# Performance work log

Measured on AMD Instinct MI355X. Metric: run time of the kernel, lower is better.

The kernel has to match this reference:

```python
import jax, jax.numpy as jnp
import numpy as np

D, H, K = 384, 6, 8
B, NQ, NK = 4, 2048, 2048
EPS = 1e-5


def _ln(x, s, b):
    m = jnp.mean(x, axis=-1, keepdims=True)
    v = jnp.mean((x - m) ** 2, axis=-1, keepdims=True)
    return (x - m) * jax.lax.rsqrt(v + EPS) * s + b


def _mha(q, k, v, Wo, bo):
    # q,k,v: [B, N, D]
    dh = D // H
    qh = q.reshape(q.shape[0], q.shape[1], H, dh).transpose(0, 2, 1, 3)
    kh = k.reshape(k.shape[0], k.shape[1], H, dh).transpose(0, 2, 1, 3)
    vh = v.reshape(v.shape[0], v.shape[1], H, dh).transpose(0, 2, 1, 3)
    scores = jnp.einsum('bhqd,bhkd->bhqk', qh, kh) / jnp.sqrt(jnp.asarray(dh, q.dtype))
    attn = jax.nn.softmax(scores, axis=-1)
    out = jnp.einsum('bhqk,bhkd->bhqd', attn, vh)
    out = out.transpose(0, 2, 1, 3).reshape(q.shape[0], q.shape[1], D)
    return out @ Wo + bo


def _knn_edge(q_coords, k_coords, q_feats, k_feats):
    # coords: [B, N, 3]; feats: [B, N, D]. EdgeConv-style feature:
    # concat(neighbor_feat - center_feat, center_feat) -> [B, Nq, K, 2D]
    d2 = (jnp.sum(q_coords ** 2, -1)[:, :, None]
          + jnp.sum(k_coords ** 2, -1)[:, None, :]
          - 2.0 * jnp.einsum('bqc,bkc->bqk', q_coords, k_coords))
    _, idx = jax.lax.top_k(-d2, K)  # [B, Nq, K] nearest neighbors in key set
    neigh = jax.vmap(lambda f, i: f[i])(k_feats, idx)  # [B, Nq, K, D]
    center = jnp.broadcast_to(q_feats[:, :, None, :], neigh.shape)
    return jnp.concatenate([neigh - center, center], axis=-1)


def setup_inputs() -> dict:
    key = jax.random.key(0)
    ks = jax.random.split(key, 24)
    s = 0.02
    return {
        'query_points': jax.random.normal(ks[0], (B, 3 + D, NQ), jnp.float32),
        'key_points': jax.random.normal(ks[1], (B, 3 + D, NK), jnp.float32),
        'ln_in_s': jnp.ones((D,), jnp.float32), 'ln_in_b': jnp.zeros((D,), jnp.float32),
        'qkv_W': jax.random.normal(ks[2], (D, 3 * D), jnp.float32) * s,
        'attn_out_W': jax.random.normal(ks[3], (D, D), jnp.float32) * s,
        'attn_out_b': jnp.zeros((D,), jnp.float32),
        'ff_W1': jax.random.normal(ks[4], (D, 2 * D), jnp.float32) * s,
        'ff_b1': jnp.zeros((2 * D,), jnp.float32),
        'ff_W2': jax.random.normal(ks[5], (2 * D, D), jnp.float32) * s,
        'ff_b2': jnp.zeros((D,), jnp.float32),
        'ffn_s': jnp.ones((D,), jnp.float32), 'ffn_b': jnp.zeros((D,), jnp.float32),
        'knn1_W': jax.random.normal(ks[6], (2 * D, D), jnp.float32) * s,
        'knn1_b': jnp.zeros((D,), jnp.float32),
        'knn2_W': jax.random.normal(ks[7], (2 * D, D), jnp.float32) * s,
        'knn2_b': jnp.zeros((D,), jnp.float32),
        'self_merge_W': jax.random.normal(ks[8], (2 * D, D), jnp.float32) * s,
        'self_merge_b': jnp.zeros((D,), jnp.float32),
        'cross_merge_W': jax.random.normal(ks[9], (2 * D, D), jnp.float32) * s,
        'cross_merge_b': jnp.zeros((D,), jnp.float32),
        'cnq_s': jnp.ones((D,), jnp.float32), 'cnq_b': jnp.zeros((D,), jnp.float32),
        'cnk_s': jnp.ones((D,), jnp.float32), 'cnk_b': jnp.zeros((D,), jnp.float32),
        'cq_W': jax.random.normal(ks[10], (D, D), jnp.float32) * s,
        'ck_W': jax.random.normal(ks[11], (D, D), jnp.float32) * s,
        'cv_W': jax.random.normal(ks[12], (D, D), jnp.float32) * s,
    }


def reference(query_points, key_points, ln_in_s, ln_in_b, qkv_W, attn_out_W,
              attn_out_b, ff_W1, ff_b1, ff_W2, ff_b2, ffn_s, ffn_b,
              knn1_W, knn1_b, knn2_W, knn2_b, self_merge_W, self_merge_b,
              cross_merge_W, cross_merge_b, cnq_s, cnq_b, cnk_s, cnk_b,
              cq_W, ck_W, cv_W):
    qp = jnp.transpose(query_points, (0, 2, 1))  # [B, Nq, 3+D]
    kp = jnp.transpose(key_points, (0, 2, 1))    # [B, Nk, 3+D]
    q_coords, q_feats = qp[..., :3], qp[..., 3:]
    k_coords, k_feats = kp[..., :3], kp[..., 3:]

    # --- self attention + self kNN geometry ---
    norm_f = _ln(q_feats, ln_in_s, ln_in_b)
    qkv = norm_f @ qkv_W
    q, k, v = jnp.split(qkv, 3, axis=-1)
    attn_f = _mha(q, k, v, attn_out_W, attn_out_b)

    edge = _knn_edge(q_coords, q_coords, norm_f, norm_f)          # [B,Nq,K,2D]
    geom = jax.nn.leaky_relu(edge @ knn1_W + knn1_b, 0.2)
    geom = jnp.max(geom, axis=2)                                   # [B,Nq,D]

    attn_f = jnp.concatenate([attn_f, geom], axis=-1) @ self_merge_W + self_merge_b
    q_feats = attn_f + q_feats

    # --- cross attention + cross kNN geometry ---
    nq = _ln(q_feats, cnq_s, cnq_b)
    nk = _ln(k_feats, cnk_s, cnk_b)
    cross_f = _mha(nq @ cq_W, nk @ ck_W, nk @ cv_W, attn_out_W, attn_out_b)

    cedge = _knn_edge(q_coords, k_coords, nq, nk)                  # [B,Nq,K,2D]
    cgeom = jax.nn.leaky_relu(cedge @ knn2_W + knn2_b, 0.2)
    cgeom = jnp.max(cgeom, axis=2)

    cross_f = jnp.concatenate([cross_f, cgeom], axis=-1) @ cross_merge_W + cross_merge_b
    q_feats = q_feats + cross_f

    # --- feed forward ---
    h = _ln(q_feats, ffn_s, ffn_b)
    q_feats = q_feats + (jax.nn.gelu(h @ ff_W1 + ff_b1) @ ff_W2 + ff_b2)

    out = jnp.concatenate([q_coords, q_feats], axis=-1)
    return jnp.transpose(out, (0, 2, 1))  # [B, 3+D, Nq]
```

## Files before the change

kernel.cpp:

```cpp
#include <hip/hip_runtime.h>
#include <cstdint>
#include <cstddef>

#define NB 4
#define NN 2048
#define DD 384
#define NH 6

typedef float f4 __attribute__((ext_vector_type(4)));
typedef float f32x4 __attribute__((ext_vector_type(4)));
typedef short bf16x8 __attribute__((ext_vector_type(8)));
typedef unsigned u32x2 __attribute__((ext_vector_type(2)));

__device__ __forceinline__ float gelu_t(float x) {
  float x3 = x*x*x;
  return 0.5f*x*(1.0f + tanhf(0.7978845608028654f*(x + 0.044715f*x3)));
}

__device__ __forceinline__ unsigned short f2b(float f) {
  unsigned u = __builtin_bit_cast(unsigned, f);
  u += 0x7fffu + ((u >> 16) & 1u);
  return (unsigned short)(u >> 16);
}

__device__ __forceinline__ float b2f(unsigned short u) {
  return __builtin_bit_cast(float, ((unsigned)u) << 16);
}

__device__ __forceinline__ unsigned cvtpk(float a, float b) {
  unsigned r;
  asm("v_cvt_pk_bf16_f32 %0, %1, %2" : "=v"(r) : "v"(a), "v"(b));
  return r;
}

typedef __attribute__((address_space(1))) const void gvoid_t;
typedef __attribute__((address_space(3))) void lvoid_t;
__device__ __forceinline__ void gl16(const void* g, void* l) {
  __builtin_amdgcn_global_load_lds((gvoid_t*)g, (lvoid_t*)l, 16, 0, 0);
}

__device__ __forceinline__ unsigned long long shfl_xor_u64(unsigned long long v, int m) {
  unsigned lo = (unsigned)v, hi = (unsigned)(v >> 32);
  lo = (unsigned)__shfl_xor((int)lo, m);
  hi = (unsigned)__shfl_xor((int)hi, m);
  return ((unsigned long long)hi << 32) | lo;
}

__global__ __launch_bounds__(256) void split_k(const float* __restrict__ pts,
                                               float* __restrict__ coords,
                                               float* __restrict__ feats) {
  __shared__ float t[32][33];
  int b = blockIdx.z;
  int c0 = blockIdx.x*32, n0 = blockIdx.y*32;
  int tx = threadIdx.x, ty = threadIdx.y;
#pragma unroll
  for (int i = 0; i < 4; ++i) {
    int c = c0 + ty + i*8;
    if (c < 387) t[ty+i*8][tx] = pts[((size_t)b*387 + c)*NN + n0 + tx];
  }
  __syncthreads();
#pragma unroll
  for (int i = 0; i < 4; ++i) {
    int n = n0 + ty + i*8;
    int c = c0 + tx;
    if (c < 387) {
      float v = t[tx][ty+i*8];
      if (c < 3) coords[((size_t)b*NN + n)*4 + c] = v;
      else       feats[((size_t)b*NN + n)*DD + (c-3)] = v;
    }
  }
}

__global__ __launch_bounds__(256) void kprep_k(float* __restrict__ c4) {
  int i = blockIdx.x*256 + threadIdx.x;
  f4 v = *(f4*)(c4 + (size_t)i*4);
  v[3] = v[0]*v[0] + v[1]*v[1] + v[2]*v[2];
  *(f4*)(c4 + (size_t)i*4) = v;
}

__global__ __launch_bounds__(256) void pack_k(const float* __restrict__ coords,
                                              const float* __restrict__ feats,
                                              float* __restrict__ out) {
  __shared__ float t[32][33];
  int b = blockIdx.z;
  int c0 = blockIdx.x*32, n0 = blockIdx.y*32;
  int tx = threadIdx.x, ty = threadIdx.y;
#pragma unroll
  for (int i = 0; i < 4; ++i) {
    int n = n0 + ty + i*8;
    int c = c0 + tx;
    if (c < 387) {
      float v = (c < 3) ? coords[((size_t)b*NN + n)*4 + c]
                        : feats[((size_t)b*NN + n)*DD + (c-3)];
      t[tx][ty+i*8] = v;
    }
  }
  __syncthreads();
#pragma unroll
  for (int i = 0; i < 4; ++i) {
    int c = c0 + ty + i*8;
    if (c < 387) out[((size_t)b*387 + c)*NN + n0 + tx] = t[ty+i*8][tx];
  }
}

__device__ __forceinline__ void ln_body(const float* __restrict__ x,
                                        const float* __restrict__ g,
                                        const float* __restrict__ bb,
                                        unsigned short* __restrict__ o,
                                        int row) {
  int lane = threadIdx.x & 63;
  const float* xr = x + (size_t)row*DD;
  float v[6]; float s = 0.f;
#pragma unroll
  for (int i = 0; i < 6; ++i) { v[i] = xr[lane + i*64]; s += v[i]; }
#pragma unroll
  for (int off = 1; off < 64; off <<= 1) s += __shfl_xor(s, off);
  float mean = s * (1.f/384.f);
  float s2 = 0.f;
#pragma unroll
  for (int i = 0; i < 6; ++i) { float d = v[i] - mean; s2 += d*d; }
#pragma unroll
  for (int off = 1; off < 64; off <<= 1) s2 += __shfl_xor(s2, off);
  float rs = rsqrtf(s2*(1.f/384.f) + 1e-5f);
  unsigned short* orow = o + (size_t)row*DD;
#pragma unroll
  for (int i = 0; i < 6; ++i) {
    int c = lane + i*64;
    orow[c] = f2b((v[i]-mean)*rs*g[c] + bb[c]);
  }
}

__global__ __launch_bounds__(256) void ln_k(const float* __restrict__ x,
                                            const float* __restrict__ g,
                                            const float* __restrict__ bb,
                                            unsigned short* __restrict__ o) {
  ln_body(x, g, bb, o, blockIdx.x*4 + (threadIdx.x >> 6));
}

__global__ __launch_bounds__(256) void ln2_k(const float* __restrict__ x1,
                                             const float* __restrict__ g1,
                                             const float* __restrict__ b1,
                                             unsigned short* __restrict__ o1,
                                             const float* __restrict__ x2,
                                             const float* __restrict__ g2,
                                             const float* __restrict__ b2,
                                             unsigned short* __restrict__ o2) {
  int row = blockIdx.x*4 + (threadIdx.x >> 6);
  if (blockIdx.y == 0) ln_body(x1, g1, b1, o1, row);
  else                 ln_body(x2, g2, b2, o2, row);
}

struct WSrcs { const float* p[13]; };

__global__ __launch_bounds__(256) void wtrans_k(WSrcs srcs, unsigned short* __restrict__ dst) {
  constexpr int KK[13]  = {384,384,384,384,768,384,384,384,384,384,768,384,768};
  constexpr int NW[13]  = {1152,384,384,384,384,384,384,384,384,384,384,768,384};
  constexpr int MD[13]  = {0,0,2,0,0,0,0,0,0,2,0,0,0};
  constexpr int OFF[13] = {0,442368,589824,737280,884736,1179648,1327104,1474560,
                           1622016,1769472,1916928,2211840,2506752};
  constexpr int PFX[14] = {0,432,576,720,864,1152,1296,1440,1584,1728,1872,2160,2448,2736};
  int bid = blockIdx.x;
  int e = 0;
  while (bid >= PFX[e+1]) ++e;
  int t = bid - PFX[e];
  int K = KK[e], N = NW[e];
  int ntiles = N >> 5;
  int kt = t / ntiles, nt = t - kt*ntiles;
  const float* src = srcs.p[e];
  __shared__ float T[32][33];
  int tx = threadIdx.x & 31, ty = threadIdx.x >> 5;
  int n = nt*32 + tx;
#pragma unroll
  for (int i = 0; i < 4; ++i) {
    int k = kt*32 + ty + i*8;
    float v = src[(size_t)k*N + n];
    if (MD[e] == 2) v = src[(size_t)(k+384)*N + n] - v;
    T[ty+i*8][tx] = v;
  }
  __syncthreads();
#pragma unroll
  for (int i = 0; i < 4; ++i) {
    int nn = nt*32 + ty + i*8;
    int kk = kt*32 + tx;
    dst[(size_t)OFF[e] + (size_t)nn*K + kk] = f2b(T[tx][ty+i*8]);
  }
}

template<int ACT, int ACC, int OB, int HALFM>
__global__ __launch_bounds__(256) void mgemm_k(const unsigned short* __restrict__ A, int lda,
                                               const unsigned short* __restrict__ Wt,
                                               const float* __restrict__ bias,
                                               void* __restrict__ Cv, int ldc, int cofs,
                                               int Kd) {
  constexpr int BM   = HALFM ? 64 : 128;
  constexpr int MT   = HALFM ? 2 : 4;
  constexpr int AG   = HALFM ? 2 : 4;
  constexpr int ABUF = BM*128;
  constexpr int BUFSZ = ABUF + 8192;
  __shared__ char lds[2*BUFSZ];
  int tid = threadIdx.x;
  int lane = tid & 63, w = tid >> 6, g = lane >> 4, c = lane & 15;
  int wr = w >> 1, wc = w & 1;
  int m0 = blockIdx.y*BM, n0 = blockIdx.x*64;
  int lrow = lane >> 3;
  int cswz = ((lane & 7) ^ lrow)*8;

  f32x4 acc[MT][2];
#pragma unroll
  for (int mt = 0; mt < MT; ++mt)
#pragma unroll
    for (int nt = 0; nt < 2; ++nt) acc[mt][nt] = 0.f;

  int KT = Kd >> 6;
  {
    char* As = lds; char* Bs = lds + ABUF;
#pragma unroll
    for (int i = 0; i < AG; ++i) {
      int rb = i*32 + w*8;
      gl16(A + (size_t)(m0 + rb + lrow)*lda + cswz, As + rb*128);
    }
#pragma unroll
    for (int i = 0; i < 2; ++i) {
      int rb = i*32 + w*8;
      gl16(Wt + (size_t)(n0 + rb + lrow)*Kd + cswz, Bs + rb*128);
    }
  }
  __syncthreads();

  for (int kt = 0; kt < KT; ++kt) {
    char* Asc = lds + (kt & 1)*BUFSZ;
    char* Bsc = Asc + ABUF;
    if (kt + 1 < KT) {
      char* Asn = lds + ((kt + 1) & 1)*BUFSZ;
      char* Bsn = Asn + ABUF;
      int k0 = (kt + 1)*64;
#pragma unroll
      for (int i = 0; i < AG; ++i) {
        int rb = i*32 + w*8;
        gl16(A + (size_t)(m0 + rb + lrow)*lda + k0 + cswz, Asn + rb*128);
      }
#pragma unroll
      for (int i = 0; i < 2; ++i) {
        int rb = i*32 + w*8;
        gl16(Wt + (size_t)(n0 + rb + lrow)*Kd + k0 + cswz, Bsn + rb*128);
      }
    }
#pragma unroll
    for (int kb = 0; kb < 2; ++kb) {
      bf16x8 af[MT], bfr[2];
#pragma unroll
      for (int mt = 0; mt < MT; ++mt) {
        int row = wr*(BM/2) + mt*16 + c;
        int ch = (kb*4 + g) ^ (row & 7);
        af[mt] = *(const bf16x8*)(Asc + row*128 + ch*16);
      }
#pragma unroll
      for (int nt = 0; nt < 2; ++nt) {
        int row = wc*32 + nt*16 + c;
        int ch = (kb*4 + g) ^ (row & 7);
        bfr[nt] = *(const bf16x8*)(Bsc + row*128 + ch*16);
      }
#pragma unroll
      for (int mt = 0; mt < MT; ++mt)
#pragma unroll
        for (int nt = 0; nt < 2; ++nt)
          acc[mt][nt] = __builtin_amdgcn_mfma_f32_16x16x32_bf16(af[mt], bfr[nt], acc[mt][nt], 0, 0, 0);
    }
    __syncthreads();
  }

#pragma unroll
  for (int mt = 0; mt < MT; ++mt) {
#pragma unroll
    for (int nt = 0; nt < 2; ++nt) {
      int coln = n0 + wc*32 + nt*16 + c;
      float bval = bias ? bias[coln] : 0.f;
#pragma unroll
      for (int r = 0; r < 4; ++r) {
        int m = m0 + wr*(BM/2) + mt*16 + 4*g + r;
        float t = acc[mt][nt][r] + bval;
        if (ACT == 1) t = gelu_t(t);
        if (OB) {
          ((unsigned short*)Cv)[(size_t)m*ldc + cofs + coln] = f2b(t);
        } else {
          float* cp = (float*)Cv + (size_t)m*ldc + cofs + coln;
          if (ACC) t += *cp;
          *cp = t;
        }
      }
    }
  }
}

struct FSegs {
  const unsigned short* A[5];
  unsigned short* out[5];
  int ldc[5];
  int cofs[5];
};

__global__ __launch_bounds__(256) void fgemm_k(FSegs fs, const unsigned short* __restrict__ Wt) {
  __shared__ char lds[49152];
  int tid = threadIdx.x;
  int lane = tid & 63, w = tid >> 6, g = lane >> 4, c = lane & 15;
  int wr = w >> 1, wc = w & 1;
  int m0 = blockIdx.y*128, n0 = blockIdx.x*64;
  int seg = n0 / 384;
  const unsigned short* A = fs.A[seg];
  int lrow = lane >> 3;
  int cswz = ((lane & 7) ^ lrow)*8;

  f32x4 acc[4][2];
#pragma unroll
  for (int mt = 0; mt < 4; ++mt)
#pragma unroll
    for (int nt = 0; nt < 2; ++nt) acc[mt][nt] = 0.f;

  {
    char* As = lds; char* Bs = lds + 16384;
#pragma unroll
    for (int i = 0; i < 4; ++i) {
      int rb = i*32 + w*8;
      gl16(A + (size_t)(m0 + rb + lrow)*384 + cswz, As + rb*128);
    }
#pragma unroll
    for (int i = 0; i < 2; ++i) {
      int rb = i*32 + w*8;
      gl16(Wt + (size_t)(n0 + rb + lrow)*384 + cswz, Bs + rb*128);
    }
  }
  __syncthreads();

  for (int kt = 0; kt < 6; ++kt) {
    char* Asc = lds + (kt & 1)*24576;
    char* Bsc = Asc + 16384;
    if (kt + 1 < 6) {
      char* Asn = lds + ((kt + 1) & 1)*24576;
      char* Bsn = Asn + 16384;
      int k0 = (kt + 1)*64;
#pragma unroll
      for (int i = 0; i < 4; ++i) {
        int rb = i*32 + w*8;
        gl16(A + (size_t)(m0 + rb + lrow)*384 + k0 + cswz, Asn + rb*128);
      }
#pragma unroll
      for (int i = 0; i < 2; ++i) {
        int rb = i*32 + w*8;
        gl16(Wt + (size_t)(n0 + rb + lrow)*384 + k0 + cswz, Bsn + rb*128);
      }
    }
#pragma unroll
    for (int kb = 0; kb < 2; ++kb) {
      bf16x8 af[4], bfr[2];
#pragma unroll
      for (int mt = 0; mt < 4; ++mt) {
        int row = wr*64 + mt*16 + c;
        int ch = (kb*4 + g) ^ (row & 7);
        af[mt] = *(const bf16x8*)(Asc + row*128 + ch*16);
      }
#pragma unroll
      for (int nt = 0; nt < 2; ++nt) {
        int row = wc*32 + nt*16 + c;
        int ch = (kb*4 + g) ^ (row & 7);
        bfr[nt] = *(const bf16x8*)(Bsc + row*128 + ch*16);
      }
#pragma unroll
      for (int mt = 0; mt < 4; ++mt)
#pragma unroll
        for (int nt = 0; nt < 2; ++nt)
          acc[mt][nt] = __builtin_amdgcn_mfma_f32_16x16x32_bf16(af[mt], bfr[nt], acc[mt][nt], 0, 0, 0);
    }
    __syncthreads();
  }

  if (seg == 2) {
    unsigned short* vtp = fs.out[2];
    int bb = m0 >> 11;
    int tokb = (m0 & 2047) + wr*64 + 4*g;
#pragma unroll
    for (int mt = 0; mt < 4; ++mt) {
#pragma unroll
      for (int nt = 0; nt < 2; ++nt) {
        int cseg = (n0 - 768) + wc*32 + nt*16 + c;
        int h = cseg >> 6, d = cseg & 63;
        u32x2 pv;
        pv[0] = cvtpk(acc[mt][nt][0], acc[mt][nt][1]);
        pv[1] = cvtpk(acc[mt][nt][2], acc[mt][nt][3]);
        *(u32x2*)(vtp + ((size_t)((bb*NH + h)*64 + d))*NN + tokb + mt*16) = pv;
      }
    }
    return;
  }

  unsigned short* outp = fs.out[seg];
  int ldcs = fs.ldc[seg];
  int cbase = fs.cofs[seg] + (n0 - seg*384);
#pragma unroll
  for (int mt = 0; mt < 4; ++mt) {
#pragma unroll
    for (int nt = 0; nt < 2; ++nt) {
      int coln = cbase + wc*32 + nt*16 + c;
#pragma unroll
      for (int r = 0; r < 4; ++r) {
        int m = m0 + wr*64 + mt*16 + 4*g + r;
        outp[(size_t)m*ldcs + coln] = f2b(acc[mt][nt][r]);
      }
    }
  }
}

__global__ __launch_bounds__(256) void flashm_k(const unsigned short* __restrict__ qkvb,
                                                const unsigned short* __restrict__ vt,
                                                unsigned short* __restrict__ o) {
  __shared__ char smem[40960];
  char* PT = smem + 32768;
  int bid = blockIdx.x;
  int s = (bid & 7)*96 + (bid >> 3);
  int qt = s & 31; int hb = s >> 5;
  int h = hb % NH, b = hb / NH;
  int q0 = qt*64;
  int tid = threadIdx.x;
  int w = tid >> 6, lane = tid & 63, g = lane >> 4, c = lane & 15;
  int lrow = lane >> 3;
  int gsw = ((lane & 7) ^ lrow)*8;

  const unsigned short* kbase = qkvb + (size_t)b*NN*1152 + 384 + h*64;
  const unsigned short* vbase = vt + ((size_t)(b*NH + h))*64*NN;

  bf16x8 qf[2];
  {
    const unsigned short* qrow = qkvb + ((size_t)(b*NN + q0 + w*16 + c))*1152 + h*64;
    qf[0] = *(const bf16x8*)(qrow + 8*g);
    qf[1] = *(const bf16x8*)(qrow + 32 + 8*g);
  }
  f32x4 oacc[4];
#pragma unroll
  for (int i = 0; i < 4; ++i) oacc[i] = 0.f;
  float lsum = 0.f;

#define FSTAGE(bf, ktb) { \
    char* KB = smem + (bf)*16384; char* VB = KB + 8192; \
    gl16(kbase + (size_t)((ktb) + w*16 + lrow)*1152 + gsw,     KB + (w*16)*128); \
    gl16(kbase + (size_t)((ktb) + w*16 + 8 + lrow)*1152 + gsw, KB + (w*16+8)*128); \
    gl16(vbase + (size_t)(w*16 + lrow)*NN + (ktb) + gsw,       VB + (w*16)*128); \
    gl16(vbase + (size_t)(w*16 + 8 + lrow)*NN + (ktb) + gsw,   VB + (w*16+8)*128); }

  FSTAGE(0, 0);
  __syncthreads();

  for (int kt = 0; kt < 32; ++kt) {
    if (kt + 1 < 32) FSTAGE((kt + 1) & 1, (kt + 1)*64);
    char* KTc = smem + (kt & 1)*16384;
    char* VTc = KTc + 8192;

    f32x4 sT[4];
#pragma unroll
    for (int nt = 0; nt < 4; ++nt) sT[nt] = 0.f;
#pragma unroll
    for (int nt = 0; nt < 4; ++nt) {
      int krow = nt*16 + c;
#pragma unroll
      for (int kb = 0; kb < 2; ++kb) {
        int ch = ((kb*4 + g) ^ (krow & 7))*16;
        bf16x8 kf_ = *(const bf16x8*)(KTc + krow*128 + ch);
        sT[nt] = __builtin_amdgcn_mfma_f32_16x16x32_bf16(kf_, qf[kb], sT[nt], 0, 0, 0);
      }
    }

    int prow = w*16 + c;
    int pswz = (c & 7) << 4;
#pragma unroll
    for (int nt = 0; nt < 4; ++nt) {
      float p0 = __builtin_amdgcn_exp2f(sT[nt][0] * 0.18033688011112042f);
      float p1 = __builtin_amdgcn_exp2f(sT[nt][1] * 0.18033688011112042f);
      float p2 = __builtin_amdgcn_exp2f(sT[nt][2] * 0.18033688011112042f);
      float p3 = __builtin_amdgcn_exp2f(sT[nt][3] * 0.18033688011112042f);
      lsum += (p0 + p1) + (p2 + p3);
      u32x2 pk;
      pk[0] = cvtpk(p0, p1);
      pk[1] = cvtpk(p2, p3);
      *(u32x2*)(PT + prow*128 + ((nt*32 + 8*g) ^ pswz)) = pk;
    }

    bf16x8 pb[2];
#pragma unroll
    for (int kb = 0; kb < 2; ++kb)
      pb[kb] = *(const bf16x8*)(PT + prow*128 + (((kb*4 + g) ^ (c & 7))*16));

#pragma unroll
    for (int dt = 0; dt < 4; ++dt) {
      int vrow = dt*16 + c;
#pragma unroll
      for (int kb = 0; kb < 2; ++kb) {
        int ch = ((kb*4 + g) ^ (vrow & 7))*16;
        bf16x8 vf = *(const bf16x8*)(VTc + vrow*128 + ch);
        oacc[dt] = __builtin_amdgcn_mfma_f32_16x16x32_bf16(vf, pb[kb], oacc[dt], 0, 0, 0);
      }
    }
    __syncthreads();
  }
#undef FSTAGE

  lsum += __shfl_xor(lsum, 16);
  lsum += __shfl_xor(lsum, 32);
  float inv = 1.f / lsum;
  size_t orow = ((size_t)b*NN + q0 + w*16 + c)*DD + h*64;
#pragma unroll
  for (int dt = 0; dt < 4; ++dt) {
    u32x2 ov;
    ov[0] = cvtpk(oacc[dt][0]*inv, oacc[dt][1]*inv);
    ov[1] = cvtpk(oacc[dt][2]*inv, oacc[dt][3]*inv);
    *(u32x2*)(o + orow + dt*16 + 4*g) = ov;
  }
}

#define CEXF(a, b) { \
  float lo_ = fminf(bf[a], bf[b]); \
  float hi_ = fmaxf(bf[a], bf[b]); \
  bf[a] = lo_; bf[b] = hi_; }

#define CEX(a, b) { \
  unsigned long long lo_ = bd[a] < bd[b] ? bd[a] : bd[b]; \
  unsigned long long hi_ = bd[a] < bd[b] ? bd[b] : bd[a]; \
  bd[a] = lo_; bd[b] = hi_; }

__global__ __launch_bounds__(256) void knn2_k(const float* __restrict__ qc4,
                                              const float* __restrict__ kc4,
                                              int* __restrict__ idx1,
                                              int* __restrict__ idx2) {
  const float* kcs = blockIdx.y ? kc4 : qc4;
  int* idxo = blockIdx.y ? idx2 : idx1;
  int lane = threadIdx.x & 63;
  int q = blockIdx.x*4 + (threadIdx.x >> 6);
  int b = q >> 11;
  f4 qv = *(const f4*)(qc4 + (size_t)q*4);
  float mx_ = -2.f*qv[0], my_ = -2.f*qv[1], mz_ = -2.f*qv[2];
  const float* kb = kcs + (size_t)b*NN*4;

  float fv[32];
  float bf[8];
#pragma unroll
  for (int i = 0; i < 8; ++i) bf[i] = INFINITY;
#pragma unroll
  for (int i = 0; i < 32; ++i) {
    f4 kv = *(const f4*)(kb + (size_t)(lane + i*64)*4);
    float f = fmaf(mx_, kv[0], fmaf(my_, kv[1], fmaf(mz_, kv[2], kv[3])));
    fv[i] = f;
#pragma unroll
    for (int k = 0; k < 8; ++k) {
      float lo = fminf(f, bf[k]);
      float hi = fmaxf(f, bf[k]);
      bf[k] = lo; f = hi;
    }
  }
#pragma unroll
  for (int m = 1; m <= 32; m <<= 1) {
    float pr[8];
#pragma unroll
    for (int i = 0; i < 8; ++i) pr[i] = __shfl_xor(bf[7-i], m);
#pragma unroll
    for (int i = 0; i < 8; ++i) bf[i] = fminf(bf[i], pr[i]);
    CEXF(0,4) CEXF(1,5) CEXF(2,6) CEXF(3,7)
    CEXF(0,2) CEXF(1,3) CEXF(4,6) CEXF(5,7)
    CEXF(0,1) CEXF(2,3) CEXF(4,5) CEXF(6,7)
  }
  float T = bf[7];

  unsigned long long bd[8];
#pragma unroll
  for (int i = 0; i < 8; ++i) bd[i] = ~0ull;
#pragma unroll
  for (int i = 0; i < 32; ++i) {
    if (__any(fv[i] <= T)) {
      unsigned u = __builtin_bit_cast(unsigned, fv[i]);
      u ^= 0x80000000u | (unsigned)((int)u >> 31);
      unsigned long long key = ((unsigned long long)u << 32) | (unsigned)(lane + i*64);
#pragma unroll
      for (int k = 0; k < 8; ++k) {
        unsigned long long lo = key < bd[k] ? key : bd[k];
        unsigned long long hi = key < bd[k] ? bd[k] : key;
        bd[k] = lo; key = hi;
      }
    }
  }
#pragma unroll
  for (int m = 1; m <= 32; m <<= 1) {
    unsigned long long pr[8];
#pragma unroll
    for (int i = 0; i < 8; ++i) pr[i] = shfl_xor_u64(bd[7-i], m);
#pragma unroll
    for (int i = 0; i < 8; ++i) bd[i] = bd[i] < pr[i] ? bd[i] : pr[i];
    CEX(0,4) CEX(1,5) CEX(2,6) CEX(3,7)
    CEX(0,2) CEX(1,3) CEX(4,6) CEX(5,7)
    CEX(0,1) CEX(2,3) CEX(4,5) CEX(6,7)
  }
  if (lane == 0) {
#pragma unroll
    for (int r = 0; r < 8; ++r) idxo[(size_t)q*8 + r] = (int)(unsigned)bd[r];
  }
}

__global__ __launch_bounds__(384) void geom_k(const unsigned short* __restrict__ GCb,
                                              const float* __restrict__ bias,
                                              const int* __restrict__ idx,
                                              unsigned short* __restrict__ out) {
  int q = blockIdx.x;
  int b = q >> 11;
  int d = threadIdx.x;
  float c = b2f(GCb[(size_t)q*768 + 384 + d]) + bias[d];
  float mx = -INFINITY;
#pragma unroll
  for (int kn = 0; kn < 8; ++kn) {
    int j = idx[(size_t)q*8 + kn];
    float gg = b2f(GCb[((size_t)(b << 11) + j)*768 + d]);
    float y = gg + c;
    y = (y > 0.f) ? y : 0.2f*y;
    mx = fmaxf(mx, y);
  }
  out[(size_t)q*768 + 384 + d] = f2b(mx);
}

extern "C" void kernel_launch(void* const* d_in, const int* in_sizes, int n_in,
                              void* d_out, int out_size, void* d_ws, size_t ws_size,
                              hipStream_t stream) {
  (void)in_sizes; (void)n_in; (void)out_size; (void)ws_size;
  const float* qpts  = (const float*)d_in[0];
  const float* kpts  = (const float*)d_in[1];
  const float* ln_s  = (const float*)d_in[2];
  const float* ln_b  = (const float*)d_in[3];
  const float* qkvW  = (const float*)d_in[4];
  const float* Wo    = (const float*)d_in[5];
  const float* bo    = (const float*)d_in[6];
  const float* ffW1  = (const float*)d_in[7];
  const float* ffb1  = (const float*)d_in[8];
  const float* ffW2  = (const float*)d_in[9];
  const float* ffb2  = (const float*)d_in[10];
  const float* ffns  = (const float*)d_in[11];
  const float* ffnb  = (const float*)d_in[12];
  const float* knn1W = (const float*)d_in[13];
  const float* knn1b = (const float*)d_in[14];
  const float* knn2W = (const float*)d_in[15];
  const float* knn2b = (const float*)d_in[16];
  const float* smW   = (const float*)d_in[17];
  const float* smb   = (const float*)d_in[18];
  const float* cmW   = (const float*)d_in[19];
  const float* cmb   = (const float*)d_in[20];
  const float* cnqs  = (const float*)d_in[21];
  const float* cnqb  = (const float*)d_in[22];
  const float* cnks  = (const float*)d_in[23];
  const float* cnkb  = (const float*)d_in[24];
  const float* cqW   = (const float*)d_in[25];
  const float* ckW   = (const float*)d_in[26];
  const float* cvW   = (const float*)d_in[27];

  float* ws = (float*)d_ws;
  float* qc4  = ws;
  float* kc4  = qc4 + 32768;
  float* qf   = kc4 + 32768;
  float* kf   = qf + 3145728;
  unsigned short* nrmb = (unsigned short*)(kf + 3145728);
  unsigned short* nkb  = (unsigned short*)(kf + 3145728 + 1572864);
  float* qkv = kf + 3145728 + 1572864 + 1572864;
  unsigned short* qkvb   = (unsigned short*)qkv;
  unsigned short* attnGb = (unsigned short*)qkv;
  unsigned short* vtb    = (unsigned short*)(qkv + 4718592);
  unsigned short* wtb    = (unsigned short*)(qkv + 4718592 + 1572864);
  unsigned short* attnOb = (unsigned short*)(qkv + 4718592 + 1572864 + 1400832);
  unsigned short* GCbb   = (unsigned short*)((float*)attnOb + 1572864);
  int* idx1 = (int*)((float*)GCbb + 3145728);
  int* idx2 = idx1 + 65536;

  const int W_FA=0, W_WO=737280, W_SM=884736, W_FB=1179648,
            W_CM=1916928, W_FF1=2211840, W_FF2=2506752;

  WSrcs srcs;
  srcs.p[0]=qkvW; srcs.p[1]=knn1W; srcs.p[2]=knn1W; srcs.p[3]=Wo; srcs.p[4]=smW;
  srcs.p[5]=cqW; srcs.p[6]=ckW; srcs.p[7]=cvW; srcs.p[8]=knn2W; srcs.p[9]=knn2W;
  srcs.p[10]=cmW; srcs.p[11]=ffW1; srcs.p[12]=ffW2;
  wtrans_k<<<2736, 256, 0, stream>>>(srcs, wtb);

  dim3 tgrid(13, 64, NB), tblk(32, 8);
  split_k<<<tgrid, tblk, 0, stream>>>(qpts, qc4, qf);
  split_k<<<tgrid, tblk, 0, stream>>>(kpts, kc4, kf);
  kprep_k<<<64, 256, 0, stream>>>(qc4);

  knn2_k<<<dim3(2048, 2), 256, 0, stream>>>(qc4, kc4, idx1, idx2);

  dim3 mg384h(6, 128), mg768(12, 64), fg(30, 64);

  ln_k<<<2048, 256, 0, stream>>>(qf, ln_s, ln_b, nrmb);
  {
    FSegs fa;
    for (int s = 0; s < 5; ++s) fa.A[s] = nrmb;
    fa.out[0] = qkvb; fa.ldc[0] = 1152; fa.cofs[0] = 0;
    fa.out[1] = qkvb; fa.ldc[1] = 1152; fa.cofs[1] = 384;
    fa.out[2] = vtb;  fa.ldc[2] = 0;    fa.cofs[2] = 0;
    fa.out[3] = GCbb; fa.ldc[3] = 768;  fa.cofs[3] = 0;
    fa.out[4] = GCbb; fa.ldc[4] = 768;  fa.cofs[4] = 384;
    fgemm_k<<<fg, 256, 0, stream>>>(fa, wtb + W_FA);
  }
  flashm_k<<<768, 256, 0, stream>>>(qkvb, vtb, attnOb);
  mgemm_k<0,0,1,1><<<mg384h, 256, 0, stream>>>(attnOb, DD, wtb+W_WO, bo, attnGb, 768, 0, DD);
  geom_k<<<8192, 384, 0, stream>>>(GCbb, knn1b, idx1, attnGb);
  mgemm_k<0,1,0,1><<<mg384h, 256, 0, stream>>>(attnGb, 768, wtb+W_SM, smb, qf, DD, 0, 768);

  ln2_k<<<dim3(2048, 2), 256, 0, stream>>>(qf, cnqs, cnqb, nrmb, kf, cnks, cnkb, nkb);
  {
    FSegs fb;
    fb.A[0] = nrmb; fb.A[1] = nkb; fb.A[2] = nkb; fb.A[3] = nkb; fb.A[4] = nrmb;
    fb.out[0] = qkvb; fb.ldc[0] = 1152; fb.cofs[0] = 0;
    fb.out[1] = qkvb; fb.ldc[1] = 1152; fb.cofs[1] = 384;
    fb.out[2] = vtb;  fb.ldc[2] = 0;    fb.cofs[2] = 0;
    fb.out[3] = GCbb; fb.ldc[3] = 768;  fb.cofs[3] = 0;
    fb.out[4] = GCbb; fb.ldc[4] = 768;  fb.cofs[4] = 384;
    fgemm_k<<<fg, 256, 0, stream>>>(fb, wtb + W_FB);
  }
  flashm_k<<<768, 256, 0, stream>>>(qkvb, vtb, attnOb);
  mgemm_k<0,0,1,1><<<mg384h, 256, 0, stream>>>(attnOb, DD, wtb+W_WO, bo, attnGb, 768, 0, DD);
  geom_k<<<8192, 384, 0, stream>>>(GCbb, knn2b, idx2, attnGb);
  mgemm_k<0,1,0,1><<<mg384h, 256, 0, stream>>>(attnGb, 768, wtb+W_CM, cmb, qf, DD, 0, 768);

  ln_k<<<2048, 256, 0, stream>>>(qf, ffns, ffnb, nrmb);
  mgemm_k<1,0,1,0><<<mg768, 256, 0, stream>>>(nrmb, DD, wtb+W_FF1, ffb1, attnGb, 768, 0, DD);
  mgemm_k<0,1,0,1><<<mg384h, 256, 0, stream>>>(attnGb, 768, wtb+W_FF2, ffb2, qf, DD, 0, 768);

  pack_k<<<tgrid, tblk, 0, stream>>>(qc4, qf, (float*)d_out);
}
```

Before: 352.1 us.

## Co-schedule kNN with fused GEMM and Wo-GEMM with geometry gather in shared launches

Folds the coordinate squared-norm prep into the split kernel. Merges the kNN search blocks into the first fused projection GEMM launch, and the output-projection GEMM with the edge-geometry max-gather, using interleaved block-index dispatch. The goal is fewer launches and letting independent latency-bound and compute-bound work overlap on the GPU. The cost is larger LDS per block for the kNN and geometry blocks, which may lower their occupancy. The geometry body now runs on 256 threads covering 384 channels, so some threads do a second pass.

```diff
diff --git a/kernel.cpp b/kernel.cpp
--- a/kernel.cpp
+++ b/kernel.cpp
@@ -68,14 +68,11 @@
       if (c < 3) coords[((size_t)b*NN + n)*4 + c] = v;
       else       feats[((size_t)b*NN + n)*DD + (c-3)] = v;
     }
-  }
-}
-
-__global__ __launch_bounds__(256) void kprep_k(float* __restrict__ c4) {
-  int i = blockIdx.x*256 + threadIdx.x;
-  f4 v = *(f4*)(c4 + (size_t)i*4);
-  v[3] = v[0]*v[0] + v[1]*v[1] + v[2]*v[2];
-  *(f4*)(c4 + (size_t)i*4) = v;
+    if (c0 == 0 && tx == 3) {
+      float x = t[0][ty+i*8], y = t[1][ty+i*8], z = t[2][ty+i*8];
+      coords[((size_t)b*NN + n)*4 + 3] = x*x + y*y + z*z;
+    }
+  }
 }
 
 __global__ __launch_bounds__(256) void pack_k(const float* __restrict__ coords,
@@ -187,21 +184,20 @@
 }
 
 template<int ACT, int ACC, int OB, int HALFM>
-__global__ __launch_bounds__(256) void mgemm_k(const unsigned short* __restrict__ A, int lda,
-                                               const unsigned short* __restrict__ Wt,
-                                               const float* __restrict__ bias,
-                                               void* __restrict__ Cv, int ldc, int cofs,
-                                               int Kd) {
+__device__ __forceinline__ void mgemm_body(const unsigned short* __restrict__ A, int lda,
+                                           const unsigned short* __restrict__ Wt,
+                                           const float* __restrict__ bias,
+                                           void* __restrict__ Cv, int ldc, int cofs,
+                                           int Kd, int bx, int by, char* lds) {
   constexpr int BM   = HALFM ? 64 : 128;
   constexpr int MT   = HALFM ? 2 : 4;
   constexpr int AG   = HALFM ? 2 : 4;
   constexpr int ABUF = BM*128;
   constexpr int BUFSZ = ABUF + 8192;
-  __shared__ char lds[2*BUFSZ];
   int tid = threadIdx.x;
   int lane = tid & 63, w = tid >> 6, g = lane >> 4, c = lane & 15;
   int wr = w >> 1, wc = w & 1;
-  int m0 = blockIdx.y*BM, n0 = blockIdx.x*64;
+  int m0 = by*BM, n0 = bx*64;
   int lrow = lane >> 3;
   int cswz = ((lane & 7) ^ lrow)*8;
 
@@ -292,6 +288,18 @@
   }
 }
 
+template<int ACT, int ACC, int OB, int HALFM>
+__global__ __launch_bounds__(256) void mgemm_k(const unsigned short* __restrict__ A, int lda,
+                                               const unsigned short* __restrict__ Wt,
+                                               const float* __restrict__ bias,
+                                               void* __restrict__ Cv, int ldc, int cofs,
+                                               int Kd) {
+  constexpr int BM = HALFM ? 64 : 128;
+  __shared__ char lds[2*(BM*128 + 8192)];
+  mgemm_body<ACT,ACC,OB,HALFM>(A, lda, Wt, bias, Cv, ldc, cofs, Kd,
+                               blockIdx.x, blockIdx.y, lds);
+}
+
 struct FSegs {
   const unsigned short* A[5];
   unsigned short* out[5];
@@ -299,12 +307,12 @@
   int cofs[5];
 };
 
-__global__ __launch_bounds__(256) void fgemm_k(FSegs fs, const unsigned short* __restrict__ Wt) {
-  __shared__ char lds[49152];
+__device__ __forceinline__ void fgemm_body(const FSegs& fs, const unsigned short* __restrict__ Wt,
+                                           int bx, int by, char* lds) {
   int tid = threadIdx.x;
   int lane = tid & 63, w = tid >> 6, g = lane >> 4, c = lane & 15;
   int wr = w >> 1, wc = w & 1;
-  int m0 = blockIdx.y*128, n0 = blockIdx.x*64;
+  int m0 = by*128, n0 = bx*64;
   int seg = n0 / 384;
   const unsigned short* A = fs.A[seg];
   int lrow = lane >> 3;
@@ -407,6 +415,171 @@
       }
     }
   }
+}
+
+__global__ __launch_bounds__(256) void fgemm_k(FSegs fs, const unsigned short* __restrict__ Wt) {
+  __shared__ char lds[49152];
+  fgemm_body(fs, Wt, blockIdx.x, blockIdx.y, lds);
+}
+
+#define CEXF(a, b) { \
+  float lo_ = fminf(bf[a], bf[b]); \
+  float hi_ = fmaxf(bf[a], bf[b]); \
+  bf[a] = lo_; bf[b] = hi_; }
+
+#define CEX(a, b) { \
+  unsigned long long lo_ = bd[a] < bd[b] ? bd[a] : bd[b]; \
+  unsigned long long hi_ = bd[a] < bd[b] ? bd[b] : bd[a]; \
+  bd[a] = lo_; bd[b] = hi_; }
+
+__device__ void knn_body(const float* __restrict__ qc4,
+                         const float* __restrict__ kcs,
+                         int* __restrict__ idxo, int bx) {
+  int lane = threadIdx.x & 63;
+  int q = bx*4 + (threadIdx.x >> 6);
+  int b = q >> 11;
+  f4 qv = *(const f4*)(qc4 + (size_t)q*4);
+  float mx_ = -2.f*qv[0], my_ = -2.f*qv[1], mz_ = -2.f*qv[2];
+  const float* kb = kcs + (size_t)b*NN*4;
+
+  float fv[32];
+  float bf[8];
+#pragma unroll
+  for (int i = 0; i < 8; ++i) bf[i] = INFINITY;
+#pragma unroll
+  for (int i = 0; i < 32; ++i) {
+    f4 kv = *(const f4*)(kb + (size_t)(lane + i*64)*4);
+    float f = fmaf(mx_, kv[0], fmaf(my_, kv[1], fmaf(mz_, kv[2], kv[3])));
+    fv[i] = f;
+#pragma unroll
+    for (int k = 0; k < 8; ++k) {
+      float lo = fminf(f, bf[k]);
+      float hi = fmaxf(f, bf[k]);
+      bf[k] = lo; f = hi;
+    }
+  }
+#pragma unroll
+  for (int m = 1; m <= 32; m <<= 1) {
+    float pr[8];
+#pragma unroll
+    for (int i = 0; i < 8; ++i) pr[i] = __shfl_xor(bf[7-i], m);
+#pragma unroll
+    for (int i = 0; i < 8; ++i) bf[i] = fminf(bf[i], pr[i]);
+    CEXF(0,4) CEXF(1,5) CEXF(2,6) CEXF(3,7)
+    CEXF(0,2) CEXF(1,3) CEXF(4,6) CEXF(5,7)
+    CEXF(0,1) CEXF(2,3) CEXF(4,5) CEXF(6,7)
+  }
+  float T = bf[7];
+
+  unsigned long long bd[8];
+#pragma unroll
+  for (int i = 0; i < 8; ++i) bd[i] = ~0ull;
+#pragma unroll
+  for (int i = 0; i < 32; ++i) {
+    if (__any(fv[i] <= T)) {
+      unsigned u = __builtin_bit_cast(unsigned, fv[i]);
+      u ^= 0x80000000u | (unsigned)((int)u >> 31);
+      unsigned long long key = ((unsigned long long)u << 32) | (unsigned)(lane + i*64);
+#pragma unroll
+      for (int k = 0; k < 8; ++k) {
+        unsigned long long lo = key < bd[k] ? key : bd[k];
+        unsigned long long hi = key < bd[k] ? bd[k] : key;
+        bd[k] = lo; key = hi;
+      }
+    }
+  }
+#pragma unroll
+  for (int m = 1; m <= 32; m <<= 1) {
+    unsigned long long pr[8];
+#pragma unroll
+    for (int i = 0; i < 8; ++i) pr[i] = shfl_xor_u64(bd[7-i], m);
+#pragma unroll
+    for (int i = 0; i < 8; ++i) bd[i] = bd[i] < pr[i] ? bd[i] : pr[i];
+    CEX(0,4) CEX(1,5) CEX(2,6) CEX(3,7)
+    CEX(0,2) CEX(1,3) CEX(4,6) CEX(5,7)
+    CEX(0,1) CEX(2,3) CEX(4,5) CEX(6,7)
+  }
+  if (lane == 0) {
+#pragma unroll
+    for (int r = 0; r < 8; ++r) idxo[(size_t)q*8 + r] = (int)(unsigned)bd[r];
+  }
+}
+
+__global__ __launch_bounds__(256) void fgknn_k(FSegs fs, const unsigned short* __restrict__ Wt,
+                                               const float* __restrict__ qc4,
+                                               const float* __restrict__ kc4,
+                                               int* __restrict__ idx1,
+                                               int* __restrict__ idx2) {
+  __shared__ char lds[49152];
+  int bid = blockIdx.x;
+  int kb;
+  if (bid < 5760) {
+    int t = bid / 3, r = bid - t*3;
+    if (r == 0) { fgemm_body(fs, Wt, t % 30, t / 30, lds); return; }
+    kb = t*2 + (r - 1);
+  } else {
+    kb = 3840 + (bid - 5760);
+  }
+  knn_body(qc4, (kb >= 2048) ? kc4 : qc4, (kb >= 2048) ? idx2 : idx1, kb & 2047);
+}
+
+__device__ __forceinline__ void geom_body(const unsigned short* __restrict__ GCb,
+                                          const float* __restrict__ bias,
+                                          const int* __restrict__ idx,
+                                          unsigned short* __restrict__ out,
+                                          int q) {
+  int b = q >> 11;
+  int t = threadIdx.x;
+  int j[8];
+#pragma unroll
+  for (int k = 0; k < 8; ++k) j[k] = idx[(size_t)q*8 + k];
+  const unsigned short* base = GCb + ((size_t)(b << 11))*768;
+  {
+    float c = b2f(GCb[(size_t)q*768 + 384 + t]) + bias[t];
+    float mx = -INFINITY;
+#pragma unroll
+    for (int k = 0; k < 8; ++k) {
+      float y = b2f(base[(size_t)j[k]*768 + t]) + c;
+      y = (y > 0.f) ? y : 0.2f*y;
+      mx = fmaxf(mx, y);
+    }
+    out[(size_t)q*768 + 384 + t] = f2b(mx);
+  }
+  if (t < 128) {
+    int d = t + 256;
+    float c = b2f(GCb[(size_t)q*768 + 384 + d]) + bias[d];
+    float mx = -INFINITY;
+#pragma unroll
+    for (int k = 0; k < 8; ++k) {
+      float y = b2f(base[(size_t)j[k]*768 + d]) + c;
+      y = (y > 0.f) ? y : 0.2f*y;
+      mx = fmaxf(mx, y);
+    }
+    out[(size_t)q*768 + 384 + d] = f2b(mx);
+  }
+}
+
+__global__ __launch_bounds__(256) void wog_k(const unsigned short* __restrict__ A,
+                                             const unsigned short* __restrict__ Wt,
+                                             const float* __restrict__ wob,
+                                             unsigned short* __restrict__ attnG,
+                                             const unsigned short* __restrict__ GCb,
+                                             const float* __restrict__ gbias,
+                                             const int* __restrict__ idx) {
+  __shared__ char lds[32768];
+  int bid = blockIdx.x;
+  int gq;
+  if (bid < 8448) {
+    int t = bid / 11, r = bid - t*11;
+    if (r == 0) {
+      mgemm_body<0,0,1,1>(A, 384, Wt, wob, attnG, 768, 0, 384, t % 6, t / 6, lds);
+      return;
+    }
+    gq = t*10 + (r - 1);
+  } else {
+    gq = 7680 + (bid - 8448);
+  }
+  geom_body(GCb, gbias, idx, attnG, gq);
 }
 
 __global__ __launch_bounds__(256) void flashm_k(const unsigned short* __restrict__ qkvb,
@@ -512,112 +685,6 @@
     ov[1] = cvtpk(oacc[dt][2]*inv, oacc[dt][3]*inv);
     *(u32x2*)(o + orow + dt*16 + 4*g) = ov;
   }
-}
-
-#define CEXF(a, b) { \
-  float lo_ = fminf(bf[a], bf[b]); \
-  float hi_ = fmaxf(bf[a], bf[b]); \
-  bf[a] = lo_; bf[b] = hi_; }
-
-#define CEX(a, b) { \
-  unsigned long long lo_ = bd[a] < bd[b] ? bd[a] : bd[b]; \
-  unsigned long long hi_ = bd[a] < bd[b] ? bd[b] : bd[a]; \
-  bd[a] = lo_; bd[b] = hi_; }
-
-__global__ __launch_bounds__(256) void knn2_k(const float* __restrict__ qc4,
-                                              const float* __restrict__ kc4,
-                                              int* __restrict__ idx1,
-                                              int* __restrict__ idx2) {
-  const float* kcs = blockIdx.y ? kc4 : qc4;
-  int* idxo = blockIdx.y ? idx2 : idx1;
-  int lane = threadIdx.x & 63;
-  int q = blockIdx.x*4 + (threadIdx.x >> 6);
-  int b = q >> 11;
-  f4 qv = *(const f4*)(qc4 + (size_t)q*4);
-  float mx_ = -2.f*qv[0], my_ = -2.f*qv[1], mz_ = -2.f*qv[2];
-  const float* kb = kcs + (size_t)b*NN*4;
-
-  float fv[32];
-  float bf[8];
-#pragma unroll
-  for (int i = 0; i < 8; ++i) bf[i] = INFINITY;
-#pragma unroll
-  for (int i = 0; i < 32; ++i) {
-    f4 kv = *(const f4*)(kb + (size_t)(lane + i*64)*4);
-    float f = fmaf(mx_, kv[0], fmaf(my_, kv[1], fmaf(mz_, kv[2], kv[3])));
-    fv[i] = f;
-#pragma unroll
-    for (int k = 0; k < 8; ++k) {
-      float lo = fminf(f, bf[k]);
-      float hi = fmaxf(f, bf[k]);
-      bf[k] = lo; f = hi;
-    }
-  }
-#pragma unroll
-  for (int m = 1; m <= 32; m <<= 1) {
-    float pr[8];
-#pragma unroll
-    for (int i = 0; i < 8; ++i) pr[i] = __shfl_xor(bf[7-i], m);
-#pragma unroll
-    for (int i = 0; i < 8; ++i) bf[i] = fminf(bf[i], pr[i]);
-    CEXF(0,4) CEXF(1,5) CEXF(2,6) CEXF(3,7)
-    CEXF(0,2) CEXF(1,3) CEXF(4,6) CEXF(5,7)
-    CEXF(0,1) CEXF(2,3) CEXF(4,5) CEXF(6,7)
-  }
-  float T = bf[7];
-
-  unsigned long long bd[8];
-#pragma unroll
-  for (int i = 0; i < 8; ++i) bd[i] = ~0ull;
-#pragma unroll
-  for (int i = 0; i < 32; ++i) {
-    if (__any(fv[i] <= T)) {
-      unsigned u = __builtin_bit_cast(unsigned, fv[i]);
-      u ^= 0x80000000u | (unsigned)((int)u >> 31);
-      unsigned long long key = ((unsigned long long)u << 32) | (unsigned)(lane + i*64);
-#pragma unroll
-      for (int k = 0; k < 8; ++k) {
-        unsigned long long lo = key < bd[k] ? key : bd[k];
-        unsigned long long hi = key < bd[k] ? bd[k] : key;
-        bd[k] = lo; key = hi;
-      }
-    }
-  }
-#pragma unroll
-  for (int m = 1; m <= 32; m <<= 1) {
-    unsigned long long pr[8];
-#pragma unroll
-    for (int i = 0; i < 8; ++i) pr[i] = shfl_xor_u64(bd[7-i], m);
-#pragma unroll
-    for (int i = 0; i < 8; ++i) bd[i] = bd[i] < pr[i] ? bd[i] : pr[i];
-    CEX(0,4) CEX(1,5) CEX(2,6) CEX(3,7)
-    CEX(0,2) CEX(1,3) CEX(4,6) CEX(5,7)
-    CEX(0,1) CEX(2,3) CEX(4,5) CEX(6,7)
-  }
-  if (lane == 0) {
-#pragma unroll
-    for (int r = 0; r < 8; ++r) idxo[(size_t)q*8 + r] = (int)(unsigned)bd[r];
-  }
-}
-
-__global__ __launch_bounds__(384) void geom_k(const unsigned short* __restrict__ GCb,
-                                              const float* __restrict__ bias,
-                                              const int* __restrict__ idx,
-                                              unsigned short* __restrict__ out) {
-  int q = blockIdx.x;
-  int b = q >> 11;
-  int d = threadIdx.x;
-  float c = b2f(GCb[(size_t)q*768 + 384 + d]) + bias[d];
-  float mx = -INFINITY;
-#pragma unroll
-  for (int kn = 0; kn < 8; ++kn) {
-    int j = idx[(size_t)q*8 + kn];
-    float gg = b2f(GCb[((size_t)(b << 11) + j)*768 + d]);
-    float y = gg + c;
-    y = (y > 0.f) ? y : 0.2f*y;
-    mx = fmaxf(mx, y);
-  }
-  out[(size_t)q*768 + 384 + d] = f2b(mx);
 }
 
 extern "C" void kernel_launch(void* const* d_in, const int* in_sizes, int n_in,
@@ -682,9 +749,6 @@
   dim3 tgrid(13, 64, NB), tblk(32, 8);
   split_k<<<tgrid, tblk, 0, stream>>>(qpts, qc4, qf);
   split_k<<<tgrid, tblk, 0, stream>>>(kpts, kc4, kf);
-  kprep_k<<<64, 256, 0, stream>>>(qc4);
-
-  knn2_k<<<dim3(2048, 2), 256, 0, stream>>>(qc4, kc4, idx1, idx2);
 
   dim3 mg384h(6, 128), mg768(12, 64), fg(30, 64);
 
@@ -697,11 +761,10 @@
     fa.out[2] = vtb;  fa.ldc[2] = 0;    fa.cofs[2] = 0;
     fa.out[3] = GCbb; fa.ldc[3] = 768;  fa.cofs[3] = 0;
     fa.out[4] = GCbb; fa.ldc[4] = 768;  fa.cofs[4] = 384;
-    fgemm_k<<<fg, 256, 0, stream>>>(fa, wtb + W_FA);
+    fgknn_k<<<6016, 256, 0, stream>>>(fa, wtb + W_FA, qc4, kc4, idx1, idx2);
   }
   flashm_k<<<768, 256, 0, stream>>>(qkvb, vtb, attnOb);
-  mgemm_k<0,0,1,1><<<mg384h, 256, 0, stream>>>(attnOb, DD, wtb+W_WO, bo, attnGb, 768, 0, DD);
-  geom_k<<<8192, 384, 0, stream>>>(GCbb, knn1b, idx1, attnGb);
+  wog_k<<<8960, 256, 0, stream>>>(attnOb, wtb+W_WO, bo, attnGb, GCbb, knn1b, idx1);
   mgemm_k<0,1,0,1><<<mg384h, 256, 0, stream>>>(attnGb, 768, wtb+W_SM, smb, qf, DD, 0, 768);
 
   ln2_k<<<dim3(2048, 2), 256, 0, stream>>>(qf, cnqs, cnqb, nrmb, kf, cnks, cnkb, nkb);
@@ -716,8 +779,7 @@
     fgemm_k<<<fg, 256, 0, stream>>>(fb, wtb + W_FB);
   }
   flashm_k<<<768, 256, 0, stream>>>(qkvb, vtb, attnOb);
-  mgemm_k<0,0,1,1><<<mg384h, 256, 0, stream>>>(attnOb, DD, wtb+W_WO, bo, attnGb, 768, 0, DD);
-  geom_k<<<8192, 384, 0, stream>>>(GCbb, knn2b, idx2, attnGb);
+  wog_k<<<8960, 256, 0, stream>>>(attnOb, wtb+W_WO, bo, attnGb, GCbb, knn2b, idx2);
   mgemm_k<0,1,0,1><<<mg384h, 256, 0, stream>>>(attnGb, 768, wtb+W_CM, cmb, qf, DD, 0, 768);
 
   ln_k<<<2048, 256, 0, stream>>>(qf, ffns, ffnb, nrmb);
```

Result: slower. 361.4 us (+2.6%).

## Rework kNN top-k selection with lane-min threshold and ballot compaction

Applied to the files above, without the earlier changes.

The kNN kernel stops keeping a per-lane sorted top-8 insertion list and per-lane merge networks. It now takes each lane's minimum distance, bitonic-sorts those minima across the wave, and uses the 8th smallest as a threshold. Candidates at or below the threshold are compacted into shared memory with ballot/popcount and sorted with one 64-wide bitonic sort on packed keys. The squared-norm prep kernel is also folded into the coordinate split kernel, removing one launch. The risk is that more than 64 candidates can pass the threshold (ties or dense clusters), in which case the extra ones are dropped silently.

```diff
diff --git a/kernel.cpp b/kernel.cpp
--- a/kernel.cpp
+++ b/kernel.cpp
@@ -68,14 +68,11 @@
       if (c < 3) coords[((size_t)b*NN + n)*4 + c] = v;
       else       feats[((size_t)b*NN + n)*DD + (c-3)] = v;
     }
-  }
-}
-
-__global__ __launch_bounds__(256) void kprep_k(float* __restrict__ c4) {
-  int i = blockIdx.x*256 + threadIdx.x;
-  f4 v = *(f4*)(c4 + (size_t)i*4);
-  v[3] = v[0]*v[0] + v[1]*v[1] + v[2]*v[2];
-  *(f4*)(c4 + (size_t)i*4) = v;
+    if (c0 == 0 && tx == 3) {
+      float x = t[0][ty+i*8], y = t[1][ty+i*8], z = t[2][ty+i*8];
+      coords[((size_t)b*NN + n)*4 + 3] = x*x + y*y + z*z;
+    }
+  }
 }
 
 __global__ __launch_bounds__(256) void pack_k(const float* __restrict__ coords,
@@ -514,90 +511,78 @@
   }
 }
 
-#define CEXF(a, b) { \
-  float lo_ = fminf(bf[a], bf[b]); \
-  float hi_ = fmaxf(bf[a], bf[b]); \
-  bf[a] = lo_; bf[b] = hi_; }
-
-#define CEX(a, b) { \
-  unsigned long long lo_ = bd[a] < bd[b] ? bd[a] : bd[b]; \
-  unsigned long long hi_ = bd[a] < bd[b] ? bd[b] : bd[a]; \
-  bd[a] = lo_; bd[b] = hi_; }
-
 __global__ __launch_bounds__(256) void knn2_k(const float* __restrict__ qc4,
                                               const float* __restrict__ kc4,
                                               int* __restrict__ idx1,
                                               int* __restrict__ idx2) {
+  __shared__ unsigned long long sbuf[4][64];
   const float* kcs = blockIdx.y ? kc4 : qc4;
   int* idxo = blockIdx.y ? idx2 : idx1;
   int lane = threadIdx.x & 63;
-  int q = blockIdx.x*4 + (threadIdx.x >> 6);
+  int w = threadIdx.x >> 6;
+  int q = blockIdx.x*4 + w;
   int b = q >> 11;
   f4 qv = *(const f4*)(qc4 + (size_t)q*4);
   float mx_ = -2.f*qv[0], my_ = -2.f*qv[1], mz_ = -2.f*qv[2];
   const float* kb = kcs + (size_t)b*NN*4;
 
   float fv[32];
-  float bf[8];
-#pragma unroll
-  for (int i = 0; i < 8; ++i) bf[i] = INFINITY;
+  float fm = INFINITY;
 #pragma unroll
   for (int i = 0; i < 32; ++i) {
     f4 kv = *(const f4*)(kb + (size_t)(lane + i*64)*4);
     float f = fmaf(mx_, kv[0], fmaf(my_, kv[1], fmaf(mz_, kv[2], kv[3])));
     fv[i] = f;
-#pragma unroll
-    for (int k = 0; k < 8; ++k) {
-      float lo = fminf(f, bf[k]);
-      float hi = fmaxf(f, bf[k]);
-      bf[k] = lo; f = hi;
-    }
-  }
-#pragma unroll
-  for (int m = 1; m <= 32; m <<= 1) {
-    float pr[8];
-#pragma unroll
-    for (int i = 0; i < 8; ++i) pr[i] = __shfl_xor(bf[7-i], m);
-#pragma unroll
-    for (int i = 0; i < 8; ++i) bf[i] = fminf(bf[i], pr[i]);
-    CEXF(0,4) CEXF(1,5) CEXF(2,6) CEXF(3,7)
-    CEXF(0,2) CEXF(1,3) CEXF(4,6) CEXF(5,7)
-    CEXF(0,1) CEXF(2,3) CEXF(4,5) CEXF(6,7)
-  }
-  float T = bf[7];
-
-  unsigned long long bd[8];
-#pragma unroll
-  for (int i = 0; i < 8; ++i) bd[i] = ~0ull;
+    fm = fminf(fm, f);
+  }
+
+  {
+    float v = fm;
+#pragma unroll
+    for (int k = 2; k <= 64; k <<= 1) {
+#pragma unroll
+      for (int j = k >> 1; j >= 1; j >>= 1) {
+        float p = __shfl_xor(v, j);
+        bool tmin = (((lane & k) == 0) == ((lane & j) == 0));
+        v = tmin ? fminf(v, p) : fmaxf(v, p);
+      }
+    }
+    fm = __shfl(v, 7);
+  }
+  float T = fm;
+
+  int cnt = 0;
 #pragma unroll
   for (int i = 0; i < 32; ++i) {
-    if (__any(fv[i] <= T)) {
-      unsigned u = __builtin_bit_cast(unsigned, fv[i]);
-      u ^= 0x80000000u | (unsigned)((int)u >> 31);
-      unsigned long long key = ((unsigned long long)u << 32) | (unsigned)(lane + i*64);
-#pragma unroll
-      for (int k = 0; k < 8; ++k) {
-        unsigned long long lo = key < bd[k] ? key : bd[k];
-        unsigned long long hi = key < bd[k] ? bd[k] : key;
-        bd[k] = lo; key = hi;
-      }
-    }
-  }
-#pragma unroll
-  for (int m = 1; m <= 32; m <<= 1) {
-    unsigned long long pr[8];
-#pragma unroll
-    for (int i = 0; i < 8; ++i) pr[i] = shfl_xor_u64(bd[7-i], m);
-#pragma unroll
-    for (int i = 0; i < 8; ++i) bd[i] = bd[i] < pr[i] ? bd[i] : pr[i];
-    CEX(0,4) CEX(1,5) CEX(2,6) CEX(3,7)
-    CEX(0,2) CEX(1,3) CEX(4,6) CEX(5,7)
-    CEX(0,1) CEX(2,3) CEX(4,5) CEX(6,7)
-  }
-  if (lane == 0) {
-#pragma unroll
-    for (int r = 0; r < 8; ++r) idxo[(size_t)q*8 + r] = (int)(unsigned)bd[r];
-  }
+    bool p = fv[i] <= T;
+    unsigned long long mask = __ballot(p);
+    if (mask) {
+      if (p) {
+        int off = cnt + (int)__popcll(mask & ((1ull << lane) - 1ull));
+        unsigned u = __builtin_bit_cast(unsigned, fv[i]);
+        u ^= 0x80000000u | (unsigned)((int)u >> 31);
+        if (off < 64)
+          sbuf[w][off] = ((unsigned long long)u << 32) | (unsigned)(lane + i*64);
+      }
+      cnt += (int)__popcll(mask);
+    }
+  }
+
+  unsigned long long key = ~0ull;
+  if (lane < cnt && lane < 64) key = sbuf[w][lane];
+#pragma unroll
+  for (int k = 2; k <= 64; k <<= 1) {
+#pragma unroll
+    for (int j = k >> 1; j >= 1; j >>= 1) {
+      unsigned long long p = shfl_xor_u64(key, j);
+      bool tmin = (((lane & k) == 0) == ((lane & j) == 0));
+      bool less = key < p;
+      unsigned long long mn = less ? key : p;
+      unsigned long long mx = less ? p : key;
+      key = tmin ? mn : mx;
+    }
+  }
+  if (lane < 8) idxo[(size_t)q*8 + lane] = (int)(unsigned)key;
 }
 
 __global__ __launch_bounds__(384) void geom_k(const unsigned short* __restrict__ GCb,
@@ -682,7 +667,6 @@
   dim3 tgrid(13, 64, NB), tblk(32, 8);
   split_k<<<tgrid, tblk, 0, stream>>>(qpts, qc4, qf);
   split_k<<<tgrid, tblk, 0, stream>>>(kpts, kc4, kf);
-  kprep_k<<<64, 256, 0, stream>>>(qc4);
 
   knn2_k<<<dim3(2048, 2), 256, 0, stream>>>(qc4, kc4, idx1, idx2);
 
```

Result: faster. 317.0 us (-10.0%).
